# Kernel tuning notes

Measured on AMD Instinct MI355X. Metric: run time of the kernel, lower is better.

The kernel has to match this reference:

```python
import jax, jax.numpy as jnp
import numpy as np

BN_EPS = 1e-3  # Keras BatchNormalization default epsilon


def setup_inputs() -> dict:
    key = jax.random.key(0)
    ks = jax.random.split(key, 10)
    B, H, W, F, K = 16, 64, 64, 512, 32
    support = 1.0 / np.sqrt(K * F)
    fc_support = np.sqrt(1.0 / F)
    return {
        "inputs": jax.random.normal(ks[0], (B, H, W, F), dtype=jnp.float32),
        # Encoder params
        "codewords": jax.random.uniform(ks[1], (K, F), minval=-support, maxval=support, dtype=jnp.float32),
        "smoothing": jax.random.uniform(ks[2], (K,), minval=-1.0, maxval=0.0, dtype=jnp.float32),
        # BatchNorm (inference mode: moving stats) over feature axis of (B, K, F)
        "bn_gamma": jnp.ones((F,), dtype=jnp.float32),
        "bn_beta": jnp.zeros((F,), dtype=jnp.float32),
        "bn_mean": jnp.zeros((F,), dtype=jnp.float32),
        "bn_var": jnp.ones((F,), dtype=jnp.float32),
        # Dense layers
        "fc_enc_w": jax.random.uniform(ks[3], (F, F), minval=-fc_support, maxval=fc_support, dtype=jnp.float32),
        "fc_enc_b": jax.random.uniform(ks[4], (F,), minval=-fc_support, maxval=fc_support, dtype=jnp.float32),
        "fc_se_w": jax.random.uniform(ks[5], (F, 1), minval=-fc_support, maxval=fc_support, dtype=jnp.float32),
        "fc_se_b": jax.random.uniform(ks[6], (1,), minval=-fc_support, maxval=fc_support, dtype=jnp.float32),
    }


def _encoder(x, codewords, smoothing, bn_gamma, bn_beta, bn_mean, bn_var):
    # x: (B, H, W, F) -> feats (B, N, F)
    B, H, W, F = x.shape
    feats = x.reshape(B, H * W, F)
    # Squared residual norms without materializing (B, N, K, F):
    x2 = jnp.sum(feats * feats, axis=-1, keepdims=True)          # (B, N, 1)
    c2 = jnp.sum(codewords * codewords, axis=-1)                 # (K,)
    xc = jnp.einsum("bnf,kf->bnk", feats, codewords)             # (B, N, K)
    sqnorms = x2 - 2.0 * xc + c2                                 # (B, N, K)
    s = jax.nn.softmax(sqnorms * smoothing, axis=-1)             # (B, N, K)
    # sum_n s[b,n,k] * (x[b,n] - c[k]) = s^T x - c * sum_n s
    s_sum = jnp.sum(s, axis=1)                                   # (B, K)
    enc = jnp.einsum("bnk,bnf->bkf", s, feats) - s_sum[:, :, None] * codewords  # (B, K, F)
    # BatchNorm (inference) + ReLU, then aggregate over codewords
    enc_bn = (enc - bn_mean) * jax.lax.rsqrt(bn_var + BN_EPS) * bn_gamma + bn_beta
    return jnp.sum(jax.nn.relu(enc_bn), axis=1)                  # (B, F)


def reference(inputs, codewords, smoothing, bn_gamma, bn_beta, bn_mean, bn_var,
              fc_enc_w, fc_enc_b, fc_se_w, fc_se_b):
    enc = _encoder(inputs, codewords, smoothing, bn_gamma, bn_beta, bn_mean, bn_var)
    attn = jax.nn.sigmoid(enc @ fc_enc_w + fc_enc_b)             # (B, F)
    featuremaps_out = attn[:, None, None, :] * inputs            # (B, H, W, F)
    se_loss_out = enc @ fc_se_w + fc_se_b                        # (B, 1)
    return (featuremaps_out, se_loss_out)
```

## Files before the change

kernel.cpp:

```cpp
#include <hip/hip_runtime.h>
#include <hip/hip_bf16.h>
#include <math.h>

#define Bb   16
#define HWn  4096
#define Ff   512
#define Kk   32
#define GCH  32

typedef __attribute__((ext_vector_type(8))) short  short8;
typedef __attribute__((ext_vector_type(4))) float  f32x4;

#define WS_SSUM  0
#define WS_EOUT  512
#define WS_ATTN  (WS_EOUT + Bb * Ff)
#define WS_CWB   (WS_ATTN + Bb * Ff)
#define WS_C2    (WS_CWB + 8192)
#define WS_SM    (WS_C2 + 32)

#define SCR_PART 0
#define SCR_S    10000000
#define SCR_RED  16777216

static __device__ __forceinline__ unsigned int pack2bf(float a, float b) {
    union { __hip_bfloat162 h; unsigned int u; } p;
    p.h = __float22bfloat162_rn(make_float2(a, b));
    return p.u;
}

__global__ void prep(const float* __restrict__ cw, const float* __restrict__ smth,
                     unsigned short* __restrict__ cwb,
                     float* __restrict__ c2l2, float* __restrict__ sml2)
{
    const int t = threadIdx.x;
    const float4* c4 = (const float4*)cw;
    #pragma unroll
    for (int j = 0; j < 16; ++j) {
        const int i = t + j * 256;
        const float4 v = c4[i];
        *reinterpret_cast<uint2*>(&cwb[i * 4]) =
            make_uint2(pack2bf(v.x, v.y), pack2bf(v.z, v.w));
    }
    const int k = t >> 3, sk = t & 7;
    float p = 0.f;
    #pragma unroll
    for (int j = 0; j < 16; ++j) {
        const float4 v = c4[k * 128 + sk + j * 8];
        p = fmaf(v.x, v.x, fmaf(v.y, v.y, fmaf(v.z, v.z, fmaf(v.w, v.w, p))));
    }
    p += __shfl_xor(p, 1); p += __shfl_xor(p, 2); p += __shfl_xor(p, 4);
    if (sk == 0) {
        const float L2E = 1.4426950408889634f;
        const float sm = smth[k];
        sml2[k] = sm * L2E;
        c2l2[k] = p * sm * L2E;
    }
}

__global__ __launch_bounds__(512, 2) void softmax_pass(
    const float* __restrict__ x, const unsigned short* __restrict__ cwb,
    const float* __restrict__ c2l2, const float* __restrict__ sml2,
    unsigned short* __restrict__ s_out, float* __restrict__ s_sum)
{
    __shared__ float sm_s[32], c2_s[32];
    __shared__ float swred[8][32];

    const int tid  = threadIdx.x;
    const int wave = tid >> 6, lane = tid & 63;
    const int col  = lane & 15, g = lane >> 4;
    const int b    = blockIdx.y;
    const int n    = blockIdx.x * 128 + wave * 16 + col;

    if (tid < 32) { sm_s[tid] = sml2[tid]; c2_s[tid] = c2l2[tid]; }
    __syncthreads();

    const float4* xr = (const float4*)(x + ((size_t)b * HWn + n) * Ff) + g * 2;
    const unsigned short* a0p = cwb + col * 512 + g * 8;
    const unsigned short* a1p = a0p + 16 * 512;
    f32x4 c0 = {0.f, 0.f, 0.f, 0.f}, c1 = {0.f, 0.f, 0.f, 0.f};
    float px = 0.f;
    #pragma unroll
    for (int fs = 0; fs < 16; ++fs) {
        const float4 v0 = xr[fs * 8];
        const float4 v1 = xr[fs * 8 + 1];
        px = fmaf(v0.x, v0.x, fmaf(v0.y, v0.y, fmaf(v0.z, v0.z, fmaf(v0.w, v0.w, px))));
        px = fmaf(v1.x, v1.x, fmaf(v1.y, v1.y, fmaf(v1.z, v1.z, fmaf(v1.w, v1.w, px))));
        union { uint4 u; short8 s; } bu;
        bu.u = make_uint4(pack2bf(v0.x, v0.y), pack2bf(v0.z, v0.w),
                          pack2bf(v1.x, v1.y), pack2bf(v1.z, v1.w));
        const short8 a0 = *(const short8*)(a0p + fs * 32);
        const short8 a1 = *(const short8*)(a1p + fs * 32);
        c0 = __builtin_amdgcn_mfma_f32_16x16x32_bf16(a0, bu.s, c0, 0, 0, 0);
        c1 = __builtin_amdgcn_mfma_f32_16x16x32_bf16(a1, bu.s, c1, 0, 0, 0);
    }
    px += __shfl_xor(px, 16); px += __shfl_xor(px, 32);

    float lg[8];
    #pragma unroll
    for (int r = 0; r < 4; ++r) {
        const int k0 = g * 4 + r;
        lg[r]     = fmaf(sm_s[k0],      fmaf(-2.f, c0[r], px), c2_s[k0]);
        lg[4 + r] = fmaf(sm_s[k0 + 16], fmaf(-2.f, c1[r], px), c2_s[k0 + 16]);
    }
    float m = lg[0];
    #pragma unroll
    for (int j = 1; j < 8; ++j) m = fmaxf(m, lg[j]);
    m = fmaxf(m, __shfl_xor(m, 16)); m = fmaxf(m, __shfl_xor(m, 32));
    float e[8], sum = 0.f;
    #pragma unroll
    for (int j = 0; j < 8; ++j) { e[j] = exp2f(lg[j] - m); sum += e[j]; }
    sum += __shfl_xor(sum, 16); sum += __shfl_xor(sum, 32);
    const float inv = 1.f / sum;
    #pragma unroll
    for (int j = 0; j < 8; ++j) e[j] *= inv;

    {
        unsigned short* sp = s_out + ((size_t)b * HWn + n) * 32 + g * 4;
        *reinterpret_cast<uint2*>(sp)      = make_uint2(pack2bf(e[0], e[1]), pack2bf(e[2], e[3]));
        *reinterpret_cast<uint2*>(sp + 16) = make_uint2(pack2bf(e[4], e[5]), pack2bf(e[6], e[7]));
    }
    #pragma unroll
    for (int j = 0; j < 8; ++j) {
        float v = e[j];
        v += __shfl_xor(v, 1); v += __shfl_xor(v, 2);
        v += __shfl_xor(v, 4); v += __shfl_xor(v, 8);
        if (col == 0) swred[wave][((j & 4) << 2) + g * 4 + (j & 3)] = v;
    }
    __syncthreads();
    if (tid < 32) {
        float a = 0.f;
        #pragma unroll
        for (int w = 0; w < 8; ++w) a += swred[w][tid];
        atomicAdd(&s_sum[b * Kk + tid], a);
    }
}

__global__ __launch_bounds__(512, 2) void enc_gemm(
    const float* __restrict__ x, const unsigned short* __restrict__ s_in,
    float* __restrict__ part)
{
    __shared__ __align__(16) float s_lds[128 * 32];
    const int tid  = threadIdx.x;
    const int wave = tid >> 6, lane = tid & 63;
    const int b    = blockIdx.y, cx = blockIdx.x;
    const int n0   = cx * 128;

    {
        const uint4 v = reinterpret_cast<const uint4*>(
            s_in + ((size_t)b * HWn + n0) * 32)[tid];
        float* d = &s_lds[tid * 8];
        d[0] = __uint_as_float(v.x << 16);
        d[1] = __uint_as_float(v.x & 0xffff0000u);
        d[2] = __uint_as_float(v.y << 16);
        d[3] = __uint_as_float(v.y & 0xffff0000u);
        d[4] = __uint_as_float(v.z << 16);
        d[5] = __uint_as_float(v.z & 0xffff0000u);
        d[6] = __uint_as_float(v.w << 16);
        d[7] = __uint_as_float(v.w & 0xffff0000u);
    }
    __syncthreads();

    float acc[4][8];
    #pragma unroll
    for (int j = 0; j < 4; ++j)
        #pragma unroll
        for (int i = 0; i < 8; ++i) acc[j][i] = 0.f;

    const int kq = wave * 4;
    const float4* xp = (const float4*)(x + ((size_t)b * HWn + n0) * Ff) + lane * 2;
    #pragma unroll 4
    for (int nn = 0; nn < 128; ++nn) {
        const f32x4 sv = *(const f32x4*)&s_lds[nn * 32 + kq];
        const float4 v0 = xp[nn * 128];
        const float4 v1 = xp[nn * 128 + 1];
        const float fx[8] = {v0.x, v0.y, v0.z, v0.w, v1.x, v1.y, v1.z, v1.w};
        #pragma unroll
        for (int j = 0; j < 4; ++j) {
            const float sj = sv[j];
            #pragma unroll
            for (int i = 0; i < 8; ++i)
                acc[j][i] = fmaf(sj, fx[i], acc[j][i]);
        }
    }
    float* basep = part + (size_t)(b * GCH + cx) * (Kk * Ff) +
                   (size_t)(wave * 4) * Ff + lane * 8;
    #pragma unroll
    for (int j = 0; j < 4; ++j) {
        *reinterpret_cast<float4*>(basep + j * Ff) =
            make_float4(acc[j][0], acc[j][1], acc[j][2], acc[j][3]);
        *reinterpret_cast<float4*>(basep + j * Ff + 4) =
            make_float4(acc[j][4], acc[j][5], acc[j][6], acc[j][7]);
    }
}

__global__ void enc_red(const float* __restrict__ scr, float* __restrict__ outp)
{
    const int idx = blockIdx.x * 256 + threadIdx.x;
    const int b   = idx >> 14;
    const int rem = idx & 16383;
    const float* p = scr + (size_t)b * GCH * 16384 + rem;
    float a = 0.f;
    #pragma unroll
    for (int c = 0; c < GCH; ++c) a += p[c * 16384];
    outp[idx] = a;
}

__global__ void enc_finish(const float* __restrict__ enc_acc,
                           const float* __restrict__ s_sum,
                           const float* __restrict__ cw,
                           const float* __restrict__ gamma,
                           const float* __restrict__ beta,
                           const float* __restrict__ mean,
                           const float* __restrict__ var,
                           const float* __restrict__ se_w,
                           const float* __restrict__ se_b,
                           float* __restrict__ enc_out,
                           float* __restrict__ se_out)
{
    __shared__ float ss[Kk];
    __shared__ float red[8];
    const int b = blockIdx.x, f = threadIdx.x;
    if (f < Kk) ss[f] = s_sum[b * Kk + f];
    __syncthreads();
    const float m  = mean[f];
    const float g  = gamma[f];
    const float bt = beta[f];
    const float iv = rsqrtf(var[f] + 1e-3f);
    float a = 0.f;
    #pragma unroll 4
    for (int k = 0; k < Kk; ++k) {
        float v = enc_acc[((long)b * Kk + k) * Ff + f] - ss[k] * cw[k * Ff + f];
        v = (v - m) * iv * g + bt;
        a += fmaxf(v, 0.f);
    }
    enc_out[b * Ff + f] = a;
    float p = a * se_w[f];
    p += __shfl_down(p, 32); p += __shfl_down(p, 16); p += __shfl_down(p, 8);
    p += __shfl_down(p, 4);  p += __shfl_down(p, 2);  p += __shfl_down(p, 1);
    if ((f & 63) == 0) red[f >> 6] = p;
    __syncthreads();
    if (f == 0) {
        float t = 0.f;
        #pragma unroll
        for (int i = 0; i < 8; ++i) t += red[i];
        se_out[b] = t + se_b[0];
    }
}

__global__ void attn_fc(const float* __restrict__ enc_out,
                        const float* __restrict__ W,
                        const float* __restrict__ bias,
                        float* __restrict__ attn)
{
    __shared__ float eo[Bb][Ff];
    const int t = threadIdx.x, fg = blockIdx.x;
    #pragma unroll
    for (int j = 0; j < 4; ++j)
        reinterpret_cast<float4*>(&eo[0][0])[t + j * 512] =
            reinterpret_cast<const float4*>(enc_out)[t + j * 512];
    __syncthreads();
    const int f  = fg * 64 + (t & 63);
    const int b0 = t >> 6;
    float a0 = bias[f], a1 = bias[f];
    #pragma unroll 8
    for (int fp = 0; fp < Ff; ++fp) {
        const float w = W[fp * Ff + f];
        a0 = fmaf(eo[b0][fp],     w, a0);
        a1 = fmaf(eo[b0 + 8][fp], w, a1);
    }
    attn[b0 * Ff + f]       = 1.f / (1.f + expf(-a0));
    attn[(b0 + 8) * Ff + f] = 1.f / (1.f + expf(-a1));
}

__global__ void bcast_mul(const float4* __restrict__ x4,
                          const float* __restrict__ attn,
                          float4* __restrict__ o4)
{
    const int stride = gridDim.x * blockDim.x;
    const int total4 = Bb * HWn * Ff / 4;
    for (int i = blockIdx.x * blockDim.x + threadIdx.x; i < total4; i += stride) {
        const float4 v = x4[i];
        const int f4 = i & 127;
        const int bb = i >> 19;
        const float4 a = *reinterpret_cast<const float4*>(&attn[bb * Ff + f4 * 4]);
        o4[i] = make_float4(v.x * a.x, v.y * a.y, v.z * a.z, v.w * a.w);
    }
}

extern "C" void kernel_launch(void* const* d_in, const int* in_sizes, int n_in,
                              void* d_out, int out_size, void* d_ws, size_t ws_size,
                              hipStream_t stream)
{
    (void)in_sizes; (void)n_in; (void)out_size; (void)ws_size;
    const float* x     = (const float*)d_in[0];
    const float* cw    = (const float*)d_in[1];
    const float* smth  = (const float*)d_in[2];
    const float* gamma = (const float*)d_in[3];
    const float* beta  = (const float*)d_in[4];
    const float* mean  = (const float*)d_in[5];
    const float* var   = (const float*)d_in[6];
    const float* Wenc  = (const float*)d_in[7];
    const float* benc  = (const float*)d_in[8];
    const float* Wse   = (const float*)d_in[9];
    const float* bse   = (const float*)d_in[10];

    float* out = (float*)d_out;
    float* ws  = (float*)d_ws;
    float* ssum = ws + WS_SSUM;
    float* eout = ws + WS_EOUT;
    float* attn = ws + WS_ATTN;
    unsigned short* cwb = (unsigned short*)(ws + WS_CWB);
    float* c2l2 = ws + WS_C2;
    float* sml2 = ws + WS_SM;

    float* scr_part = out + SCR_PART;
    unsigned short* scr_s = (unsigned short*)(out + SCR_S);
    float* scr_red  = out + SCR_RED;

    hipMemsetAsync(ssum, 0, (size_t)Bb * Kk * sizeof(float), stream);
    prep<<<1, 256, 0, stream>>>(cw, smth, cwb, c2l2, sml2);
    softmax_pass<<<dim3(GCH, Bb), 512, 0, stream>>>(x, cwb, c2l2, sml2, scr_s, ssum);
    enc_gemm<<<dim3(GCH, Bb), 512, 0, stream>>>(x, scr_s, scr_part);
    enc_red<<<1024, 256, 0, stream>>>(scr_part, scr_red);
    enc_finish<<<Bb, 512, 0, stream>>>(scr_red, ssum, cw, gamma, beta, mean, var,
                                       Wse, bse, eout, out + (long)Bb * HWn * Ff);
    attn_fc<<<8, 512, 0, stream>>>(eout, Wenc, benc, attn);
    bcast_mul<<<2048, 256, 0, stream>>>((const float4*)x, attn, (float4*)out);
}
```

Measured before the change: 179.8 us.

## Fuse softmax pass and encoding GEMM into one kernel via LDS

Merges the softmax-assignment kernel and the encoding GEMM kernel into a single kernel. Softmax weights are written straight to shared memory in fp32 instead of being stored to global scratch as bf16 and reloaded. This removes one launch and a global round trip of the assignment matrix. It also lets the second read of the x tile hit in cache, and it keeps fp32 weights instead of rounding them to bf16. The cost is a longer kernel with more register and LDS use per block, which could lower occupancy.

```diff
diff --git a/kernel.cpp b/kernel.cpp
--- a/kernel.cpp
+++ b/kernel.cpp
@@ -19,7 +19,6 @@
 #define WS_SM    (WS_C2 + 32)
 
 #define SCR_PART 0
-#define SCR_S    10000000
 #define SCR_RED  16777216
 
 static __device__ __forceinline__ unsigned int pack2bf(float a, float b) {
@@ -57,74 +56,78 @@
     }
 }
 
-__global__ __launch_bounds__(512, 2) void softmax_pass(
+__global__ __launch_bounds__(512, 2) void enc_fused(
     const float* __restrict__ x, const unsigned short* __restrict__ cwb,
     const float* __restrict__ c2l2, const float* __restrict__ sml2,
-    unsigned short* __restrict__ s_out, float* __restrict__ s_sum)
-{
+    float* __restrict__ part, float* __restrict__ s_sum)
+{
+    __shared__ __align__(16) float s_lds[128 * 32];
     __shared__ float sm_s[32], c2_s[32];
     __shared__ float swred[8][32];
 
     const int tid  = threadIdx.x;
     const int wave = tid >> 6, lane = tid & 63;
     const int col  = lane & 15, g = lane >> 4;
-    const int b    = blockIdx.y;
-    const int n    = blockIdx.x * 128 + wave * 16 + col;
+    const int b    = blockIdx.y, cx = blockIdx.x;
+    const int n_loc = wave * 16 + col;
+    const int n     = cx * 128 + n_loc;
 
     if (tid < 32) { sm_s[tid] = sml2[tid]; c2_s[tid] = c2l2[tid]; }
     __syncthreads();
 
-    const float4* xr = (const float4*)(x + ((size_t)b * HWn + n) * Ff) + g * 2;
-    const unsigned short* a0p = cwb + col * 512 + g * 8;
-    const unsigned short* a1p = a0p + 16 * 512;
-    f32x4 c0 = {0.f, 0.f, 0.f, 0.f}, c1 = {0.f, 0.f, 0.f, 0.f};
-    float px = 0.f;
-    #pragma unroll
-    for (int fs = 0; fs < 16; ++fs) {
-        const float4 v0 = xr[fs * 8];
-        const float4 v1 = xr[fs * 8 + 1];
-        px = fmaf(v0.x, v0.x, fmaf(v0.y, v0.y, fmaf(v0.z, v0.z, fmaf(v0.w, v0.w, px))));
-        px = fmaf(v1.x, v1.x, fmaf(v1.y, v1.y, fmaf(v1.z, v1.z, fmaf(v1.w, v1.w, px))));
-        union { uint4 u; short8 s; } bu;
-        bu.u = make_uint4(pack2bf(v0.x, v0.y), pack2bf(v0.z, v0.w),
-                          pack2bf(v1.x, v1.y), pack2bf(v1.z, v1.w));
-        const short8 a0 = *(const short8*)(a0p + fs * 32);
-        const short8 a1 = *(const short8*)(a1p + fs * 32);
-        c0 = __builtin_amdgcn_mfma_f32_16x16x32_bf16(a0, bu.s, c0, 0, 0, 0);
-        c1 = __builtin_amdgcn_mfma_f32_16x16x32_bf16(a1, bu.s, c1, 0, 0, 0);
-    }
-    px += __shfl_xor(px, 16); px += __shfl_xor(px, 32);
-
-    float lg[8];
-    #pragma unroll
-    for (int r = 0; r < 4; ++r) {
-        const int k0 = g * 4 + r;
-        lg[r]     = fmaf(sm_s[k0],      fmaf(-2.f, c0[r], px), c2_s[k0]);
-        lg[4 + r] = fmaf(sm_s[k0 + 16], fmaf(-2.f, c1[r], px), c2_s[k0 + 16]);
-    }
-    float m = lg[0];
-    #pragma unroll
-    for (int j = 1; j < 8; ++j) m = fmaxf(m, lg[j]);
-    m = fmaxf(m, __shfl_xor(m, 16)); m = fmaxf(m, __shfl_xor(m, 32));
-    float e[8], sum = 0.f;
-    #pragma unroll
-    for (int j = 0; j < 8; ++j) { e[j] = exp2f(lg[j] - m); sum += e[j]; }
-    sum += __shfl_xor(sum, 16); sum += __shfl_xor(sum, 32);
-    const float inv = 1.f / sum;
-    #pragma unroll
-    for (int j = 0; j < 8; ++j) e[j] *= inv;
-
     {
-        unsigned short* sp = s_out + ((size_t)b * HWn + n) * 32 + g * 4;
-        *reinterpret_cast<uint2*>(sp)      = make_uint2(pack2bf(e[0], e[1]), pack2bf(e[2], e[3]));
-        *reinterpret_cast<uint2*>(sp + 16) = make_uint2(pack2bf(e[4], e[5]), pack2bf(e[6], e[7]));
-    }
-    #pragma unroll
-    for (int j = 0; j < 8; ++j) {
-        float v = e[j];
-        v += __shfl_xor(v, 1); v += __shfl_xor(v, 2);
-        v += __shfl_xor(v, 4); v += __shfl_xor(v, 8);
-        if (col == 0) swred[wave][((j & 4) << 2) + g * 4 + (j & 3)] = v;
+        const float4* xr = (const float4*)(x + ((size_t)b * HWn + n) * Ff) + g * 2;
+        const unsigned short* a0p = cwb + col * 512 + g * 8;
+        const unsigned short* a1p = a0p + 16 * 512;
+        f32x4 c0 = {0.f, 0.f, 0.f, 0.f}, c1 = {0.f, 0.f, 0.f, 0.f};
+        float px = 0.f;
+        #pragma unroll
+        for (int fs = 0; fs < 16; ++fs) {
+            const float4 v0 = xr[fs * 8];
+            const float4 v1 = xr[fs * 8 + 1];
+            px = fmaf(v0.x, v0.x, fmaf(v0.y, v0.y, fmaf(v0.z, v0.z, fmaf(v0.w, v0.w, px))));
+            px = fmaf(v1.x, v1.x, fmaf(v1.y, v1.y, fmaf(v1.z, v1.z, fmaf(v1.w, v1.w, px))));
+            union { uint4 u; short8 s; } bu;
+            bu.u = make_uint4(pack2bf(v0.x, v0.y), pack2bf(v0.z, v0.w),
+                              pack2bf(v1.x, v1.y), pack2bf(v1.z, v1.w));
+            const short8 a0 = *(const short8*)(a0p + fs * 32);
+            const short8 a1 = *(const short8*)(a1p + fs * 32);
+            c0 = __builtin_amdgcn_mfma_f32_16x16x32_bf16(a0, bu.s, c0, 0, 0, 0);
+            c1 = __builtin_amdgcn_mfma_f32_16x16x32_bf16(a1, bu.s, c1, 0, 0, 0);
+        }
+        px += __shfl_xor(px, 16); px += __shfl_xor(px, 32);
+
+        float lg[8];
+        #pragma unroll
+        for (int r = 0; r < 4; ++r) {
+            const int k0 = g * 4 + r;
+            lg[r]     = fmaf(sm_s[k0],      fmaf(-2.f, c0[r], px), c2_s[k0]);
+            lg[4 + r] = fmaf(sm_s[k0 + 16], fmaf(-2.f, c1[r], px), c2_s[k0 + 16]);
+        }
+        float m = lg[0];
+        #pragma unroll
+        for (int j = 1; j < 8; ++j) m = fmaxf(m, lg[j]);
+        m = fmaxf(m, __shfl_xor(m, 16)); m = fmaxf(m, __shfl_xor(m, 32));
+        float e[8], sum = 0.f;
+        #pragma unroll
+        for (int j = 0; j < 8; ++j) { e[j] = exp2f(lg[j] - m); sum += e[j]; }
+        sum += __shfl_xor(sum, 16); sum += __shfl_xor(sum, 32);
+        const float inv = 1.f / sum;
+        #pragma unroll
+        for (int j = 0; j < 8; ++j) e[j] *= inv;
+
+        #pragma unroll
+        for (int r = 0; r < 4; ++r) {
+            s_lds[n_loc * 32 + g * 4 + r]      = e[r];
+            s_lds[n_loc * 32 + 16 + g * 4 + r] = e[4 + r];
+        }
+        #pragma unroll
+        for (int j = 0; j < 8; ++j) {
+            float v = e[j];
+            v += __shfl_xor(v, 1); v += __shfl_xor(v, 2);
+            v += __shfl_xor(v, 4); v += __shfl_xor(v, 8);
+            if (col == 0) swred[wave][((j & 4) << 2) + g * 4 + (j & 3)] = v;
+        }
     }
     __syncthreads();
     if (tid < 32) {
@@ -133,32 +136,6 @@
         for (int w = 0; w < 8; ++w) a += swred[w][tid];
         atomicAdd(&s_sum[b * Kk + tid], a);
     }
-}
-
-__global__ __launch_bounds__(512, 2) void enc_gemm(
-    const float* __restrict__ x, const unsigned short* __restrict__ s_in,
-    float* __restrict__ part)
-{
-    __shared__ __align__(16) float s_lds[128 * 32];
-    const int tid  = threadIdx.x;
-    const int wave = tid >> 6, lane = tid & 63;
-    const int b    = blockIdx.y, cx = blockIdx.x;
-    const int n0   = cx * 128;
-
-    {
-        const uint4 v = reinterpret_cast<const uint4*>(
-            s_in + ((size_t)b * HWn + n0) * 32)[tid];
-        float* d = &s_lds[tid * 8];
-        d[0] = __uint_as_float(v.x << 16);
-        d[1] = __uint_as_float(v.x & 0xffff0000u);
-        d[2] = __uint_as_float(v.y << 16);
-        d[3] = __uint_as_float(v.y & 0xffff0000u);
-        d[4] = __uint_as_float(v.z << 16);
-        d[5] = __uint_as_float(v.z & 0xffff0000u);
-        d[6] = __uint_as_float(v.w << 16);
-        d[7] = __uint_as_float(v.w & 0xffff0000u);
-    }
-    __syncthreads();
 
     float acc[4][8];
     #pragma unroll
@@ -167,7 +144,7 @@
         for (int i = 0; i < 8; ++i) acc[j][i] = 0.f;
 
     const int kq = wave * 4;
-    const float4* xp = (const float4*)(x + ((size_t)b * HWn + n0) * Ff) + lane * 2;
+    const float4* xp = (const float4*)(x + ((size_t)b * HWn + cx * 128) * Ff) + lane * 2;
     #pragma unroll 4
     for (int nn = 0; nn < 128; ++nn) {
         const f32x4 sv = *(const f32x4*)&s_lds[nn * 32 + kq];
@@ -314,13 +291,11 @@
     float* sml2 = ws + WS_SM;
 
     float* scr_part = out + SCR_PART;
-    unsigned short* scr_s = (unsigned short*)(out + SCR_S);
     float* scr_red  = out + SCR_RED;
 
     hipMemsetAsync(ssum, 0, (size_t)Bb * Kk * sizeof(float), stream);
     prep<<<1, 256, 0, stream>>>(cw, smth, cwb, c2l2, sml2);
-    softmax_pass<<<dim3(GCH, Bb), 512, 0, stream>>>(x, cwb, c2l2, sml2, scr_s, ssum);
-    enc_gemm<<<dim3(GCH, Bb), 512, 0, stream>>>(x, scr_s, scr_part);
+    enc_fused<<<dim3(GCH, Bb), 512, 0, stream>>>(x, cwb, c2l2, sml2, scr_part, ssum);
     enc_red<<<1024, 256, 0, stream>>>(scr_part, scr_red);
     enc_finish<<<Bb, 512, 0, stream>>>(scr_red, ssum, cw, gamma, beta, mean, var,
                                        Wse, bse, eout, out + (long)Bb * HWn * Ff);
```

Measured after the change: 175.0 us. 1.03x faster.
